# Optimization experiments

Hardware: AMD Instinct MI355X
Metric: run time of the kernel (lower is better)

## Reference

```python
import jax, jax.numpy as jnp
import numpy as np

LAMBDAS = (1.0, 10.0)
MAX_NEURONS = 12
RECONFIG = 50
INIT_BATCH = 4000
BATCH_INC = 2166
NS = 2  # switch point: normal equations -> QR -> incremental QR


def setup_inputs() -> dict:
    key = jax.random.key(0)
    kx, ky = jax.random.split(key)
    X = jax.random.normal(kx, (30000, 784), dtype=jnp.float32)
    labels = jax.random.randint(ky, (30000,), 0, 10)
    Y = jax.nn.one_hot(labels, 10, dtype=jnp.float32)  # [N, 10] one-hot targets
    return {"X": X, "Y": Y}


def _forward(X, Y, key):
    N, d = X.shape
    n_cand = len(LAMBDAS) * RECONFIG
    lam = jnp.repeat(jnp.asarray(LAMBDAS, dtype=X.dtype), RECONFIG)  # [n_cand]
    H = jnp.zeros((N, MAX_NEURONS), dtype=X.dtype)
    W = jnp.zeros((d, 0), dtype=X.dtype)
    b = jnp.zeros((0,), dtype=X.dtype)
    Q = R = QT = beta = None
    y = Y
    batch_size = INIT_BATCH
    for k in range(MAX_NEURONS):
        key, kperm, kw, kb = jax.random.split(key, 4)
        indices = jax.random.permutation(kperm, N)[:batch_size]
        Xk = X[indices]              # [B, d]
        Tk = Y[indices]              # [B, 10]
        ek = Tk if k == 0 else Tk - y[indices]  # residual on the batch
        # candidate random features, scaled per-lambda
        W_random = lam * (2.0 * jax.random.uniform(kw, (d, n_cand), dtype=X.dtype) - 1.0)
        b_random = lam * (2.0 * jax.random.uniform(kb, (1, n_cand), dtype=X.dtype) - 1.0)
        h = jax.nn.sigmoid(Xk @ W_random + b_random)             # [B, n_cand]
        v = (ek.T @ h) ** 2 / jnp.sum(h * h, axis=0)             # [10, n_cand]
        best = jnp.argmax(jnp.mean(v, axis=0))
        W_c = jax.lax.dynamic_slice_in_dim(W_random, best, 1, axis=1)  # [d, 1]
        b_c = jax.lax.dynamic_slice_in_dim(b_random, best, 1, axis=1)[0]  # [1]
        h_c = jax.nn.sigmoid(X @ W_c + b_c)[:, 0]                # [N]
        H = H.at[:, k].set(h_c)
        W = jnp.concatenate([W, W_c], axis=1)
        b = jnp.concatenate([b, b_c], axis=0)
        Hk = H[:, : k + 1]
        if k < NS:
            beta = jnp.linalg.inv(Hk.T @ Hk) @ (Hk.T @ Y)
        elif k == NS:
            Q, R = jnp.linalg.qr(Hk)
            QT = Q.T @ Y
            beta = jax.scipy.linalg.solve_triangular(R, QT, lower=False)
        else:
            # incremental Gram-Schmidt QR update with the new column h_c
            r1 = Q.T @ h_c                       # [k]
            t = h_c - Q @ r1
            r2 = jnp.linalg.norm(t)
            q = t / r2
            Q = jnp.concatenate([Q, q[:, None]], axis=1)
            R = jnp.block([[R, r1[:, None]],
                           [jnp.zeros((1, k), R.dtype), r2[None, None]]])
            QT = jnp.concatenate([QT, (q @ Y)[None, :]], axis=0)
            beta = jax.scipy.linalg.solve_triangular(R, QT, lower=False)
        y = Hk @ beta
        batch_size += BATCH_INC
    return W, b, beta


def reference(X, Y):
    return _forward(X, Y, jax.random.key(42))
```

## Files before the change

kernel.cpp:

```cpp
#include <hip/hip_runtime.h>
#include <cstdint>
#include <cstddef>
#include <cmath>

#define N_ROWS 30000
#define D_IN   784
#define NC     100
#define NCP    128
#define NSEG   12
#define SEG    30000
#define SORT_BLOCKS 118
#define KP     800
#define MAXBLK 435
#define SL     16

typedef short bf16x8 __attribute__((ext_vector_type(8)));
typedef float f32x4  __attribute__((ext_vector_type(4)));

struct Hdr {
  uint32_t kperm[12][2];
  uint32_t kw[12][2];
  uint32_t kb[12][2];
  uint32_t sub[12][2][2];
  int best; int pad0;
  float bsel;
  float r2arr[12];
  float r1s[12 * SL];
  float r1bs[12 * SL];
  float R[144];
  float QT[120];
  float beta[120];
  float den[100];
  float num[1000];
};

__device__ __forceinline__ void tf2x32(uint32_t k0, uint32_t k1,
                                       uint32_t x0, uint32_t x1,
                                       uint32_t& o0, uint32_t& o1) {
  const uint32_t kx = k0 ^ k1 ^ 0x1BD11BDAu;
  x0 += k0; x1 += k1;
  x0 += x1; x1 = (x1<<13)|(x1>>19); x1 ^= x0;
  x0 += x1; x1 = (x1<<15)|(x1>>17); x1 ^= x0;
  x0 += x1; x1 = (x1<<26)|(x1>>6);  x1 ^= x0;
  x0 += x1; x1 = (x1<<6) |(x1>>26); x1 ^= x0;
  x0 += k1; x1 += kx + 1u;
  x0 += x1; x1 = (x1<<17)|(x1>>15); x1 ^= x0;
  x0 += x1; x1 = (x1<<29)|(x1>>3);  x1 ^= x0;
  x0 += x1; x1 = (x1<<16)|(x1>>16); x1 ^= x0;
  x0 += x1; x1 = (x1<<24)|(x1>>8);  x1 ^= x0;
  x0 += kx; x1 += k0 + 2u;
  x0 += x1; x1 = (x1<<13)|(x1>>19); x1 ^= x0;
  x0 += x1; x1 = (x1<<15)|(x1>>17); x1 ^= x0;
  x0 += x1; x1 = (x1<<26)|(x1>>6);  x1 ^= x0;
  x0 += x1; x1 = (x1<<6) |(x1>>26); x1 ^= x0;
  x0 += k0; x1 += k1 + 3u;
  x0 += x1; x1 = (x1<<17)|(x1>>15); x1 ^= x0;
  x0 += x1; x1 = (x1<<29)|(x1>>3);  x1 ^= x0;
  x0 += x1; x1 = (x1<<16)|(x1>>16); x1 ^= x0;
  x0 += x1; x1 = (x1<<24)|(x1>>8);  x1 ^= x0;
  x0 += k1; x1 += kx + 4u;
  x0 += x1; x1 = (x1<<13)|(x1>>19); x1 ^= x0;
  x0 += x1; x1 = (x1<<15)|(x1>>17); x1 ^= x0;
  x0 += x1; x1 = (x1<<26)|(x1>>6);  x1 ^= x0;
  x0 += x1; x1 = (x1<<6) |(x1>>26); x1 ^= x0;
  x0 += kx; x1 += k0 + 5u;
  o0 = x0; o1 = x1;
}

__device__ __forceinline__ float u01(uint32_t bits) {
  return __uint_as_float((bits >> 9) | 0x3f800000u) - 1.0f;
}

__device__ __forceinline__ uint32_t rbits32(uint32_t k0, uint32_t k1, uint32_t idx) {
  uint32_t o0, o1;
  tf2x32(k0, k1, 0u, idx, o0, o1);
  return o0 ^ o1;
}

__device__ __forceinline__ ushort f2bf_rne(float f) {
  uint32_t u = __float_as_uint(f);
  return (ushort)((u + 0x7fffu + ((u >> 16) & 1u)) >> 16);
}
__device__ __forceinline__ float bf2f(ushort h) {
  return __uint_as_float(((uint32_t)h) << 16);
}

__global__ void k_rng_chain(Hdr* h) {
  if (threadIdx.x != 0 || blockIdx.x != 0) return;
  uint32_t c0 = 0u, c1 = 42u;
  for (int k = 0; k < 12; k++) {
    uint32_t t0, t1;
    tf2x32(c0, c1, 0u, 1u, t0, t1); h->kperm[k][0] = t0; h->kperm[k][1] = t1;
    tf2x32(c0, c1, 0u, 2u, t0, t1); h->kw[k][0]   = t0; h->kw[k][1]   = t1;
    tf2x32(c0, c1, 0u, 3u, t0, t1); h->kb[k][0]   = t0; h->kb[k][1]   = t1;
    uint32_t p0 = h->kperm[k][0], p1 = h->kperm[k][1];
    for (int r = 0; r < 2; r++) {
      uint32_t s0, s1, n0, n1;
      tf2x32(p0, p1, 0u, 1u, s0, s1);
      tf2x32(p0, p1, 0u, 0u, n0, n1);
      h->sub[k][r][0] = s0; h->sub[k][r][1] = s1;
      p0 = n0; p1 = n1;
    }
    tf2x32(c0, c1, 0u, 0u, t0, t1); c0 = t0; c1 = t1;
  }
}

__global__ __launch_bounds__(256) void k_sortkeys(const Hdr* __restrict__ h,
    uint32_t* __restrict__ keys, int* __restrict__ vals, int round) {
  int p = blockIdx.x * 256 + threadIdx.x;
  if (p >= NSEG * SEG) return;
  int s = p / SEG, i = p % SEG;
  keys[p] = rbits32(h->sub[s][round][0], h->sub[s][round][1], (uint32_t)i);
  if (round == 0) vals[p] = i;
}

__global__ __launch_bounds__(256) void k_hist(const uint32_t* __restrict__ keys,
    uint32_t* __restrict__ hs, int shift) {
  __shared__ uint32_t hloc[256];
  int s = blockIdx.x / SORT_BLOCKS, b = blockIdx.x % SORT_BLOCKS;
  hloc[threadIdx.x] = 0;
  __syncthreads();
  int i = b * 256 + threadIdx.x;
  if (i < SEG) {
    uint32_t d = (keys[s * SEG + i] >> shift) & 255u;
    atomicAdd(&hloc[d], 1u);
  }
  __syncthreads();
  hs[(size_t)(s * SORT_BLOCKS + b) * 256 + threadIdx.x] = hloc[threadIdx.x];
}

__global__ __launch_bounds__(256) void k_scan(uint32_t* hs, uint32_t* baseA) {
  __shared__ uint32_t tot[256];
  __shared__ uint32_t base[256];
  int s = blockIdx.x, d = threadIdx.x;
  uint32_t run = 0;
  uint32_t buf[30];
  for (int c0 = 0; c0 < SORT_BLOCKS; c0 += 30) {
    int n = SORT_BLOCKS - c0; if (n > 30) n = 30;
    #pragma unroll
    for (int j = 0; j < 30; j++)
      if (j < n) buf[j] = hs[(size_t)(s * SORT_BLOCKS + c0 + j) * 256 + d];
    #pragma unroll
    for (int j = 0; j < 30; j++)
      if (j < n) {
        uint32_t c = buf[j];
        hs[(size_t)(s * SORT_BLOCKS + c0 + j) * 256 + d] = run;
        run += c;
      }
  }
  tot[d] = run;
  __syncthreads();
  if (d == 0) {
    uint32_t acc = 0;
    for (int q = 0; q < 256; q++) { base[q] = acc; acc += tot[q]; }
  }
  __syncthreads();
  baseA[s * 256 + d] = base[d];
}

__global__ __launch_bounds__(256) void k_scatter(const uint32_t* __restrict__ ik,
    const int* __restrict__ iv, uint32_t* __restrict__ ok, int* __restrict__ ov,
    const uint32_t* __restrict__ hs, const uint32_t* __restrict__ baseA, int shift) {
  __shared__ uint16_t wh[4][256];
  int s = blockIdx.x / SORT_BLOCKS, b = blockIdx.x % SORT_BLOCKS;
  int tid = threadIdx.x;
  for (int q = tid; q < 1024; q += 256) ((uint16_t*)wh)[q] = 0;
  __syncthreads();
  int i = b * 256 + tid;
  bool valid = (i < SEG);
  uint32_t key = 0, dg = 0; int val = 0;
  if (valid) {
    key = ik[s * SEG + i];
    val = iv[s * SEG + i];
    dg = (key >> shift) & 255u;
  }
  unsigned long long vm = __ballot(valid ? 1 : 0);
  unsigned long long m = ~0ULL;
  for (int bit = 0; bit < 8; bit++) {
    unsigned long long bm = __ballot((int)((dg >> bit) & 1u));
    m &= ((dg >> bit) & 1u) ? bm : ~bm;
  }
  m &= vm;
  int wv = tid >> 6, lane = tid & 63;
  int rw = __popcll(m & ((1ULL << lane) - 1ULL));
  if (valid && rw == 0) wh[wv][dg] = (uint16_t)__popcll(m);
  __syncthreads();
  if (valid) {
    int rank = rw;
    for (int q = 0; q < wv; q++) rank += wh[q][dg];
    uint32_t pos = hs[(size_t)(s * SORT_BLOCKS + b) * 256 + dg] + baseA[s * 256 + dg] + rank;
    ok[s * SEG + pos] = key;
    ov[s * SEG + pos] = val;
  }
}

__global__ __launch_bounds__(256) void k_gen(const Hdr* __restrict__ h,
    float* __restrict__ Wr, short* __restrict__ Wthi, short* __restrict__ Wtlo) {
  int t = blockIdx.x * 256 + threadIdx.x;
  if (t >= NSEG * NCP * KP) return;
  int seg = t / (NCP * KP);
  int r = t % (NCP * KP);
  int c = r / KP, d = r % KP;
  float val = 0.f;
  if (c < NC && d < D_IN) {
    int n = d * NC + c;
    float u = u01(rbits32(h->kw[seg][0], h->kw[seg][1], (uint32_t)n));
    float lam = (c < 50) ? 1.f : 10.f;
    val = lam * (2.f * u - 1.f);
  }
  ushort hi = f2bf_rne(val);
  ushort lo = f2bf_rne(val - bf2f(hi));
  Wthi[t] = (short)hi;
  Wtlo[t] = (short)lo;
  if (d < D_IN) Wr[(size_t)seg * D_IN * NCP + (size_t)d * NCP + c] = val;
}

__global__ __launch_bounds__(256) void k_genb(const Hdr* __restrict__ h, float* __restrict__ br) {
  int t = blockIdx.x * 256 + threadIdx.x;
  if (t >= NSEG * NC) return;
  int k = t / NC, c = t % NC;
  float u = u01(rbits32(h->kb[k][0], h->kb[k][1], (uint32_t)c));
  float lam = (c < 50) ? 1.f : 10.f;
  br[t] = lam * (2.f * u - 1.f);
}

__global__ __launch_bounds__(256) void k_batch_mfma(const float* __restrict__ X,
    const short* __restrict__ Wthi, const short* __restrict__ Wtlo,
    const float* __restrict__ br, const int* __restrict__ perm,
    const float* __restrict__ Y, const float* __restrict__ Hbuf,
    const Hdr* __restrict__ hd, float* __restrict__ P, int kk, int bs) {
  __shared__ short Ah[64][40], Al[64][40];
  __shared__ short Bh[128][40], Bl[128][40];
  __shared__ int idxs[64];
  __shared__ float ekS[64][10];
  __shared__ float hS[64][12];
  __shared__ float betaS[120];
  int tid = threadIdx.x;
  int row0 = blockIdx.x * 64;
  if (tid < 64) {
    int rr = row0 + tid;
    idxs[tid] = perm[rr < bs ? rr : (bs - 1)];
  }
  if (kk > 0 && tid < kk * 10) betaS[tid] = hd->beta[tid];
  __syncthreads();
  if (kk > 0) {
    for (int q = tid; q < 64 * kk; q += 256) {
      int r = q / kk, m = q % kk;
      hS[r][m] = Hbuf[(size_t)idxs[r] * 12 + m];
    }
  }
  __syncthreads();
  for (int q = tid; q < 640; q += 256) {
    int r = q / 10, j = q % 10;
    float e = 0.f;
    if (row0 + r < bs) {
      e = Y[(size_t)idxs[r] * 10 + j];
      if (kk > 0) {
        float yv = 0.f;
        for (int m = 0; m < kk; m++) yv += hS[r][m] * betaS[m * 10 + j];
        e -= yv;
      }
    }
    ekS[r][j] = e;
  }
  int wave = tid >> 6, lane = tid & 63;
  int kg = lane >> 4, ln = lane & 15;

  f32x4 acc[4][2];
  #pragma unroll
  for (int m = 0; m < 4; m++)
    #pragma unroll
    for (int j = 0; j < 2; j++)
      acc[m][j] = (f32x4){0.f, 0.f, 0.f, 0.f};

  int arow = tid >> 2, aq = tid & 3;
  int bcol = tid >> 1, bh2 = tid & 1;

  for (int k0 = 0; k0 < KP; k0 += 32) {
    __syncthreads();
    {
      int kbase = k0 + aq * 8;
      const float* xr = X + (size_t)idxs[arow] * D_IN;
      float v[8];
      if (kbase + 8 <= D_IN) {
        float4 p0 = *(const float4*)(xr + kbase);
        float4 p1 = *(const float4*)(xr + kbase + 4);
        v[0]=p0.x; v[1]=p0.y; v[2]=p0.z; v[3]=p0.w;
        v[4]=p1.x; v[5]=p1.y; v[6]=p1.z; v[7]=p1.w;
      } else {
        #pragma unroll
        for (int q = 0; q < 8; q++) v[q] = (kbase + q < D_IN) ? xr[kbase + q] : 0.f;
      }
      uint32_t ph[4], pl[4];
      #pragma unroll
      for (int q = 0; q < 4; q++) {
        ushort h0 = f2bf_rne(v[2*q]),   h1 = f2bf_rne(v[2*q+1]);
        ushort l0 = f2bf_rne(v[2*q]   - bf2f(h0));
        ushort l1 = f2bf_rne(v[2*q+1] - bf2f(h1));
        ph[q] = (uint32_t)h0 | ((uint32_t)h1 << 16);
        pl[q] = (uint32_t)l0 | ((uint32_t)l1 << 16);
      }
      *(uint4*)&Ah[arow][aq*8] = make_uint4(ph[0], ph[1], ph[2], ph[3]);
      *(uint4*)&Al[arow][aq*8] = make_uint4(pl[0], pl[1], pl[2], pl[3]);
    }
    {
      int boff = bh2 * 16;
      const uint4* sh = (const uint4*)(Wthi + (size_t)bcol * KP + k0 + boff);
      const uint4* sl = (const uint4*)(Wtlo + (size_t)bcol * KP + k0 + boff);
      uint4 h0 = sh[0], h1 = sh[1], l0 = sl[0], l1 = sl[1];
      *(uint4*)&Bh[bcol][boff]     = h0;
      *(uint4*)&Bh[bcol][boff + 8] = h1;
      *(uint4*)&Bl[bcol][boff]     = l0;
      *(uint4*)&Bl[bcol][boff + 8] = l1;
    }
    __syncthreads();
    bf16x8 bhf[2], blf[2];
    #pragma unroll
    for (int j = 0; j < 2; j++) {
      int n = (2 * wave + j) * 16 + ln;
      bhf[j] = *(bf16x8*)&Bh[n][kg * 8];
      blf[j] = *(bf16x8*)&Bl[n][kg * 8];
    }
    #pragma unroll
    for (int m = 0; m < 4; m++) {
      bf16x8 ah = *(bf16x8*)&Ah[m * 16 + ln][kg * 8];
      bf16x8 al = *(bf16x8*)&Al[m * 16 + ln][kg * 8];
      #pragma unroll
      for (int j = 0; j < 2; j++) {
        acc[m][j] = __builtin_amdgcn_mfma_f32_16x16x32_bf16(ah, bhf[j], acc[m][j], 0, 0, 0);
        acc[m][j] = __builtin_amdgcn_mfma_f32_16x16x32_bf16(ah, blf[j], acc[m][j], 0, 0, 0);
        acc[m][j] = __builtin_amdgcn_mfma_f32_16x16x32_bf16(al, bhf[j], acc[m][j], 0, 0, 0);
      }
    }
  }
  #pragma unroll
  for (int j = 0; j < 2; j++) {
    int col = (2 * wave + j) * 16 + ln;
    float bias = (col < NC) ? br[col] : 0.f;
    float den_t = 0.f;
    float num_t[10];
    #pragma unroll
    for (int q = 0; q < 10; q++) num_t[q] = 0.f;
    #pragma unroll
    for (int m = 0; m < 4; m++) {
      #pragma unroll
      for (int r = 0; r < 4; r++) {
        int rl = m * 16 + kg * 4 + r;
        if (row0 + rl < bs) {
          float hsig = 1.f / (1.f + expf(-(acc[m][j][r] + bias)));
          den_t += hsig * hsig;
          #pragma unroll
          for (int q = 0; q < 10; q++) num_t[q] += hsig * ekS[rl][q];
        }
      }
    }
    den_t += __shfl_xor(den_t, 16, 64);
    den_t += __shfl_xor(den_t, 32, 64);
    #pragma unroll
    for (int q = 0; q < 10; q++) {
      num_t[q] += __shfl_xor(num_t[q], 16, 64);
      num_t[q] += __shfl_xor(num_t[q], 32, 64);
    }
    if (kg == 0 && col < NC) {
      float* dst = P + (size_t)blockIdx.x * 1100 + col * 11;
      dst[0] = den_t;
      #pragma unroll
      for (int q = 0; q < 10; q++) dst[1 + q] = num_t[q];
    }
  }
}

__global__ __launch_bounds__(256) void k_score_select(const float* __restrict__ P,
    Hdr* h, const float* __restrict__ brk, const float* __restrict__ Wr,
    float* __restrict__ wcol, float* __restrict__ outW, float* __restrict__ outB,
    int* __restrict__ ticket, int k, int nblk) {
  int c = blockIdx.x;
  int tid = threadIdx.x;
  int q = tid % 11, g = tid / 11;
  float acc = 0.f;
  if (tid < 253) {
    for (int b = g; b < nblk; b += 23)
      acc += P[(size_t)b * 1100 + c * 11 + q];
  }
  __shared__ float red[23][11];
  if (tid < 253) red[g][q] = acc;
  __syncthreads();
  if (tid < 11) {
    float s = 0.f;
    #pragma unroll
    for (int g2 = 0; g2 < 23; g2++) s += red[g2][tid];
    if (tid == 0) h->den[c] = s;
    else h->num[c * 10 + tid - 1] = s;
  }
  __shared__ int sdone;
  __syncthreads();
  __threadfence();
  if (tid == 0) {
    int old = atomicAdd(ticket, 1);
    sdone = (old == NC - 1) ? 1 : 0;
  }
  __syncthreads();
  if (!sdone) return;
  __threadfence();
  __shared__ int sbest;
  if (tid < 12 * SL) { h->r1s[tid] = 0.f; h->r1bs[tid] = 0.f; }
  if (tid == 0) {
    float best = -1.f; int bi = 0;
    for (int cc = 0; cc < NC; cc++) {
      float s = 0.f;
      for (int j = 0; j < 10; j++) { float n = h->num[cc * 10 + j]; s += n * n; }
      float v = s / (h->den[cc] * 10.f);
      if (v > best) { best = v; bi = cc; }
    }
    h->best = bi;
    h->bsel = brk[bi];
    outB[k] = h->bsel;
    sbest = bi;
  }
  __syncthreads();
  int best = sbest;
  for (int d = tid; d < D_IN; d += 256) {
    float v = Wr[(size_t)d * NCP + best];
    wcol[d] = v;
    outW[d * 12 + k] = v;
  }
}

__global__ __launch_bounds__(256) void k_hc(const float* __restrict__ X,
    const Hdr* __restrict__ h, const float* __restrict__ wcol,
    float* __restrict__ H, float* __restrict__ hc, int k) {
  int lane = threadIdx.x & 63;
  int row = blockIdx.x * 4 + (threadIdx.x >> 6);
  if (row >= N_ROWS) return;
  const float4* xp = (const float4*)(X + (size_t)row * D_IN);
  const float4* wp = (const float4*)wcol;
  float acc = 0.f;
  #pragma unroll
  for (int it = 0; it < 4; it++) {
    int p = lane + it * 64;
    if (p < 196) {
      float4 xv = xp[p], wv = wp[p];
      acc += xv.x * wv.x + xv.y * wv.y + xv.z * wv.z + xv.w * wv.w;
    }
  }
  #pragma unroll
  for (int o = 32; o > 0; o >>= 1) acc += __shfl_xor(acc, o, 64);
  if (lane == 0) {
    float hv = 1.f / (1.f + expf(-(acc + h->bsel)));
    H[(size_t)row * 12 + k] = hv;
    hc[row] = hv;
  }
}

__global__ __launch_bounds__(256) void k_dotQ(const float* __restrict__ Tcm,
    const float* __restrict__ vec, float* __restrict__ dst) {
  int j = blockIdx.x / SL, sl = blockIdx.x % SL;
  const float* q = Tcm + (size_t)j * N_ROWS;
  int i0 = sl * (N_ROWS / SL);
  int i1 = i0 + (N_ROWS / SL);
  float a = 0.f;
  for (int i = i0 + threadIdx.x; i < i1; i += 256) a += q[i] * vec[i];
  __shared__ float red[256];
  red[threadIdx.x] = a;
  __syncthreads();
  for (int s = 128; s > 0; s >>= 1) {
    if (threadIdx.x < s) red[threadIdx.x] += red[threadIdx.x + s];
    __syncthreads();
  }
  if (threadIdx.x == 0) dst[j * SL + sl] = red[0];
}

__global__ __launch_bounds__(256) void k_sub_fin(Hdr* h, float* __restrict__ Tcm,
    const float* __restrict__ basev, const float* __restrict__ coefp,
    const float* __restrict__ Y, float* __restrict__ partials,
    float* __restrict__ out_beta, int* __restrict__ ticket, int k, int dofin) {
  __shared__ float cf[12];
  int tid = threadIdx.x;
  if (tid < 12) {
    float s = 0.f;
    #pragma unroll
    for (int s8 = 0; s8 < SL; s8++) s += coefp[tid * SL + s8];
    float r2j = (tid < k) ? h->r2arr[tid] : 1.f;
    cf[tid] = s / (r2j * r2j);
  }
  __syncthreads();
  int i = blockIdx.x * 256 + tid;
  float t = 0.f;
  float v[11];
  #pragma unroll
  for (int q = 0; q < 11; q++) v[q] = 0.f;
  if (i < N_ROWS) {
    t = basev[i];
    for (int j = 0; j < k; j++) t -= Tcm[(size_t)j * N_ROWS + i] * cf[j];
    Tcm[(size_t)k * N_ROWS + i] = t;
    if (dofin) {
      const float* yr = Y + (size_t)i * 10;
      #pragma unroll
      for (int q = 0; q < 10; q++) v[q] = t * yr[q];
      v[10] = t * t;
    }
  }
  if (!dofin) return;
  #pragma unroll
  for (int o = 1; o < 64; o <<= 1) {
    #pragma unroll
    for (int q = 0; q < 11; q++) v[q] += __shfl_xor(v[q], o, 64);
  }
  __shared__ float wred[4][11];
  int wave = tid >> 6, lane = tid & 63;
  if (lane == 0) {
    #pragma unroll
    for (int q = 0; q < 11; q++) wred[wave][q] = v[q];
  }
  __syncthreads();
  if (tid < 11) {
    float s = wred[0][tid] + wred[1][tid] + wred[2][tid] + wred[3][tid];
    partials[blockIdx.x * 12 + tid] = s;
  }
  __shared__ int sdone;
  __syncthreads();
  __threadfence();
  if (tid == 0) {
    int old = atomicAdd(ticket, 1);
    sdone = (old == SORT_BLOCKS - 1) ? 1 : 0;
  }
  __syncthreads();
  if (!sdone) return;
  __threadfence();
  __shared__ float red[23][11];
  int q = tid % 11, g = tid / 11;
  float acc2 = 0.f;
  if (tid < 253) {
    for (int b = g; b < SORT_BLOCKS; b += 23)
      acc2 += partials[b * 12 + q];
  }
  if (tid < 253) red[g][q] = acc2;
  __syncthreads();
  __shared__ float s[11];
  __shared__ float Rcol[12];
  __shared__ float r2s;
  if (tid < 11) {
    float ss = 0.f;
    #pragma unroll
    for (int g2 = 0; g2 < 23; g2++) ss += red[g2][tid];
    s[tid] = ss;
  }
  __syncthreads();
  if (tid == 0) {
    float r2 = sqrtf(s[10]);
    h->r2arr[k] = r2;
    h->R[k * 12 + k] = r2;
    r2s = r2;
    Rcol[k] = r2;
    for (int i2 = 0; i2 < k; i2++) {
      float rs = 0.f;
      #pragma unroll
      for (int s8 = 0; s8 < SL; s8++) rs += h->r1s[i2 * SL + s8] + h->r1bs[i2 * SL + s8];
      float Rik = rs / h->r2arr[i2];
      h->R[i2 * 12 + k] = Rik;
      Rcol[i2] = Rik;
    }
  }
  __syncthreads();
  if (tid < 10) {
    float qtk = s[tid] / r2s;
    h->QT[k * 10 + tid] = qtk;
    float bloc[12];
    for (int i2 = k; i2 >= 0; i2--) {
      float t2 = (i2 == k) ? qtk : h->QT[i2 * 10 + tid];
      for (int m = i2 + 1; m <= k; m++) {
        float Rim = (m == k) ? Rcol[i2] : h->R[i2 * 12 + m];
        t2 -= Rim * bloc[m];
      }
      t2 /= ((i2 == k) ? r2s : h->R[i2 * 12 + i2]);
      bloc[i2] = t2;
      h->beta[i2 * 10 + tid] = t2;
      out_beta[i2 * 10 + tid] = t2;
    }
  }
}

static inline int cdiv(int a, int b) { return (a + b - 1) / b; }

extern "C" void kernel_launch(void* const* d_in, const int* in_sizes, int n_in,
                              void* d_out, int out_size, void* d_ws, size_t ws_size,
                              hipStream_t stream) {
  const float* X = (const float*)d_in[0];
  const float* Y = (const float*)d_in[1];
  float* out = (float*)d_out;
  float* outW = out;
  float* outB = out + 9408;
  float* outBeta = out + 9420;

  char* base = (char*)d_ws;
  Hdr* hdr = (Hdr*)base;
  float* r1p  = (float*)(base + offsetof(Hdr, r1s));
  float* r1bp = (float*)(base + offsetof(Hdr, r1bs));

  size_t off = 16384;
  auto nxt = [&](size_t bytes) -> void* {
    void* p = base + off;
    off += (bytes + 255) & ~(size_t)255;
    return p;
  };
  int* tickets = (int*)nxt(256);
  uint32_t* keysA = (uint32_t*)nxt((size_t)NSEG * SEG * 4);
  uint32_t* keysB = (uint32_t*)nxt((size_t)NSEG * SEG * 4);
  int* valsA = (int*)nxt((size_t)NSEG * SEG * 4);
  int* valsB = (int*)nxt((size_t)NSEG * SEG * 4);
  uint32_t* hs = (uint32_t*)nxt((size_t)NSEG * SORT_BLOCKS * 256 * 4);
  uint32_t* baseA = (uint32_t*)nxt((size_t)NSEG * 256 * 4);
  float* WrAll = (float*)nxt((size_t)NSEG * D_IN * NCP * 4);
  short* WthiAll = (short*)nxt((size_t)NSEG * NCP * KP * 2);
  short* WtloAll = (short*)nxt((size_t)NSEG * NCP * KP * 2);
  float* brAll = (float*)nxt((size_t)NSEG * NC * 4);
  float* wcol = (float*)nxt((size_t)D_IN * 4);
  float* Pbuf = (float*)nxt((size_t)MAXBLK * 1100 * 4);
  float* Tcm = (float*)nxt((size_t)12 * N_ROWS * 4);
  float* Hbuf = (float*)nxt((size_t)N_ROWS * 12 * 4);
  float* hcbuf = (float*)nxt((size_t)N_ROWS * 4);
  float* partials = (float*)nxt(128 * 12 * 4);

  hipMemsetAsync(tickets, 0, 256, stream);

  k_rng_chain<<<1, 64, 0, stream>>>(hdr);

  const int keygrid = cdiv(NSEG * SEG, 256);
  const int sortgrid = NSEG * SORT_BLOCKS;
  for (int round = 0; round < 2; round++) {
    k_sortkeys<<<keygrid, 256, 0, stream>>>(hdr, keysA, valsA, round);
    for (int pass = 0; pass < 4; pass++) {
      uint32_t* ik = (pass & 1) ? keysB : keysA;
      uint32_t* ok = (pass & 1) ? keysA : keysB;
      int* iv = (pass & 1) ? valsB : valsA;
      int* ov = (pass & 1) ? valsA : valsB;
      k_hist<<<sortgrid, 256, 0, stream>>>(ik, hs, 8 * pass);
      k_scan<<<NSEG, 256, 0, stream>>>(hs, baseA);
      k_scatter<<<sortgrid, 256, 0, stream>>>(ik, iv, ok, ov, hs, baseA, 8 * pass);
    }
  }

  k_gen<<<cdiv(NSEG * NCP * KP, 256), 256, 0, stream>>>(hdr, WrAll, WthiAll, WtloAll);
  k_genb<<<cdiv(NSEG * NC, 256), 256, 0, stream>>>(hdr, brAll);

  for (int k = 0; k < 12; k++) {
    int bs = 4000 + 2166 * k;
    int nblk = cdiv(bs, 64);
    const int* perm = valsA + (size_t)k * SEG;
    const short* Wthi = WthiAll + (size_t)k * NCP * KP;
    const short* Wtlo = WtloAll + (size_t)k * NCP * KP;
    const float* brk = brAll + (size_t)k * NC;

    k_batch_mfma<<<nblk, 256, 0, stream>>>(X, Wthi, Wtlo, brk, perm, Y, Hbuf, hdr, Pbuf, k, bs);
    k_score_select<<<NC, 256, 0, stream>>>(Pbuf, hdr, brk,
        WrAll + (size_t)k * D_IN * NCP, wcol, outW, outB, &tickets[k], k, nblk);
    k_hc<<<7500, 256, 0, stream>>>(X, hdr, wcol, Hbuf, hcbuf, k);
    if (k > 0) k_dotQ<<<k * SL, 256, 0, stream>>>(Tcm, hcbuf, r1p);
    if (k == 1 || k == 2) {
      k_sub_fin<<<SORT_BLOCKS, 256, 0, stream>>>(hdr, Tcm, hcbuf, r1p, Y, partials,
          outBeta, &tickets[32 + k], k, 0);
      k_dotQ<<<k * SL, 256, 0, stream>>>(Tcm, Tcm + (size_t)k * N_ROWS, r1bp);
      k_sub_fin<<<SORT_BLOCKS, 256, 0, stream>>>(hdr, Tcm, Tcm + (size_t)k * N_ROWS, r1bp,
          Y, partials, outBeta, &tickets[32 + k], k, 1);
    } else {
      k_sub_fin<<<SORT_BLOCKS, 256, 0, stream>>>(hdr, Tcm, hcbuf, r1p, Y, partials,
          outBeta, &tickets[32 + k], k, 1);
    }
  }
}
```

Baseline: 1.647 ms.

## Presplit X to bf16 hi/lo once; fuse radix-sort key gen, histogram and scan

X is now split into bf16 hi/lo pairs once by a dedicated kernel, and the batch MFMA kernel loads those pairs directly instead of re-splitting gathered rows on every call. The radix sort merges key generation with the first histogram, and folds each per-segment scan into the histogram kernel through a last-block ticket. The bias generation kernel is merged into the weight generator. Together these remove repeated conversion arithmetic and several kernel launches, at the cost of an extra 96 MB of hi/lo buffers and threadfence/atomic ticket synchronisation.

```diff
diff --git a/kernel.cpp b/kernel.cpp
--- a/kernel.cpp
+++ b/kernel.cpp
@@ -105,34 +105,40 @@
   }
 }
 
-__global__ __launch_bounds__(256) void k_sortkeys(const Hdr* __restrict__ h,
-    uint32_t* __restrict__ keys, int* __restrict__ vals, int round) {
-  int p = blockIdx.x * 256 + threadIdx.x;
-  if (p >= NSEG * SEG) return;
-  int s = p / SEG, i = p % SEG;
-  keys[p] = rbits32(h->sub[s][round][0], h->sub[s][round][1], (uint32_t)i);
-  if (round == 0) vals[p] = i;
-}
-
-__global__ __launch_bounds__(256) void k_hist(const uint32_t* __restrict__ keys,
-    uint32_t* __restrict__ hs, int shift) {
-  __shared__ uint32_t hloc[256];
-  int s = blockIdx.x / SORT_BLOCKS, b = blockIdx.x % SORT_BLOCKS;
-  hloc[threadIdx.x] = 0;
-  __syncthreads();
-  int i = b * 256 + threadIdx.x;
-  if (i < SEG) {
-    uint32_t d = (keys[s * SEG + i] >> shift) & 255u;
-    atomicAdd(&hloc[d], 1u);
-  }
-  __syncthreads();
-  hs[(size_t)(s * SORT_BLOCKS + b) * 256 + threadIdx.x] = hloc[threadIdx.x];
-}
-
-__global__ __launch_bounds__(256) void k_scan(uint32_t* hs, uint32_t* baseA) {
+__global__ __launch_bounds__(256) void k_splitX(const float* __restrict__ X,
+    short* __restrict__ Xhi, short* __restrict__ Xlo) {
+  int t = blockIdx.x * 256 + threadIdx.x;
+  if (t >= N_ROWS * (KP / 8)) return;
+  int i = t / (KP / 8), g = t % (KP / 8);
+  int kb = g * 8;
+  float v[8];
+  if (kb + 8 <= D_IN) {
+    const float* xr = X + (size_t)i * D_IN + kb;
+    float4 p0 = *(const float4*)xr;
+    float4 p1 = *(const float4*)(xr + 4);
+    v[0]=p0.x; v[1]=p0.y; v[2]=p0.z; v[3]=p0.w;
+    v[4]=p1.x; v[5]=p1.y; v[6]=p1.z; v[7]=p1.w;
+  } else {
+    #pragma unroll
+    for (int q = 0; q < 8; q++) v[q] = 0.f;
+  }
+  uint32_t ph[4], pl[4];
+  #pragma unroll
+  for (int q = 0; q < 4; q++) {
+    ushort h0 = f2bf_rne(v[2*q]),   h1 = f2bf_rne(v[2*q+1]);
+    ushort l0 = f2bf_rne(v[2*q]   - bf2f(h0));
+    ushort l1 = f2bf_rne(v[2*q+1] - bf2f(h1));
+    ph[q] = (uint32_t)h0 | ((uint32_t)h1 << 16);
+    pl[q] = (uint32_t)l0 | ((uint32_t)l1 << 16);
+  }
+  size_t o = (size_t)i * KP + kb;
+  *(uint4*)(Xhi + o) = make_uint4(ph[0], ph[1], ph[2], ph[3]);
+  *(uint4*)(Xlo + o) = make_uint4(pl[0], pl[1], pl[2], pl[3]);
+}
+
+__device__ __forceinline__ void scan_segment(uint32_t* hs, uint32_t* baseA, int s, int d) {
   __shared__ uint32_t tot[256];
   __shared__ uint32_t base[256];
-  int s = blockIdx.x, d = threadIdx.x;
   uint32_t run = 0;
   uint32_t buf[30];
   for (int c0 = 0; c0 < SORT_BLOCKS; c0 += 30) {
@@ -156,6 +162,57 @@
   }
   __syncthreads();
   baseA[s * 256 + d] = base[d];
+}
+
+__global__ __launch_bounds__(256) void k_keys_hist(const Hdr* __restrict__ h,
+    uint32_t* __restrict__ keys, int* __restrict__ vals,
+    uint32_t* __restrict__ hs, uint32_t* __restrict__ baseA,
+    int* __restrict__ tick, int round) {
+  __shared__ uint32_t hloc[256];
+  int s = blockIdx.x / SORT_BLOCKS, b = blockIdx.x % SORT_BLOCKS;
+  int tid = threadIdx.x;
+  hloc[tid] = 0;
+  __syncthreads();
+  int i = b * 256 + tid;
+  if (i < SEG) {
+    uint32_t key = rbits32(h->sub[s][round][0], h->sub[s][round][1], (uint32_t)i);
+    keys[s * SEG + i] = key;
+    if (round == 0) vals[s * SEG + i] = i;
+    atomicAdd(&hloc[key & 255u], 1u);
+  }
+  __syncthreads();
+  hs[(size_t)(s * SORT_BLOCKS + b) * 256 + tid] = hloc[tid];
+  __shared__ int sdone;
+  __threadfence();
+  if (tid == 0) sdone = (atomicAdd(&tick[s], 1) == SORT_BLOCKS - 1) ? 1 : 0;
+  __syncthreads();
+  if (!sdone) return;
+  __threadfence();
+  scan_segment(hs, baseA, s, tid);
+}
+
+__global__ __launch_bounds__(256) void k_hist_scan(const uint32_t* __restrict__ keys,
+    uint32_t* __restrict__ hs, uint32_t* __restrict__ baseA,
+    int* __restrict__ tick, int shift) {
+  __shared__ uint32_t hloc[256];
+  int s = blockIdx.x / SORT_BLOCKS, b = blockIdx.x % SORT_BLOCKS;
+  int tid = threadIdx.x;
+  hloc[tid] = 0;
+  __syncthreads();
+  int i = b * 256 + tid;
+  if (i < SEG) {
+    uint32_t d = (keys[s * SEG + i] >> shift) & 255u;
+    atomicAdd(&hloc[d], 1u);
+  }
+  __syncthreads();
+  hs[(size_t)(s * SORT_BLOCKS + b) * 256 + tid] = hloc[tid];
+  __shared__ int sdone;
+  __threadfence();
+  if (tid == 0) sdone = (atomicAdd(&tick[s], 1) == SORT_BLOCKS - 1) ? 1 : 0;
+  __syncthreads();
+  if (!sdone) return;
+  __threadfence();
+  scan_segment(hs, baseA, s, tid);
 }
 
 __global__ __launch_bounds__(256) void k_scatter(const uint32_t* __restrict__ ik,
@@ -195,9 +252,16 @@
 }
 
 __global__ __launch_bounds__(256) void k_gen(const Hdr* __restrict__ h,
-    float* __restrict__ Wr, short* __restrict__ Wthi, short* __restrict__ Wtlo) {
+    float* __restrict__ Wr, short* __restrict__ Wthi, short* __restrict__ Wtlo,
+    float* __restrict__ br) {
   int t = blockIdx.x * 256 + threadIdx.x;
   if (t >= NSEG * NCP * KP) return;
+  if (t < NSEG * NC) {
+    int k = t / NC, c = t % NC;
+    float u = u01(rbits32(h->kb[k][0], h->kb[k][1], (uint32_t)c));
+    float lam = (c < 50) ? 1.f : 10.f;
+    br[t] = lam * (2.f * u - 1.f);
+  }
   int seg = t / (NCP * KP);
   int r = t % (NCP * KP);
   int c = r / KP, d = r % KP;
@@ -215,16 +279,8 @@
   if (d < D_IN) Wr[(size_t)seg * D_IN * NCP + (size_t)d * NCP + c] = val;
 }
 
-__global__ __launch_bounds__(256) void k_genb(const Hdr* __restrict__ h, float* __restrict__ br) {
-  int t = blockIdx.x * 256 + threadIdx.x;
-  if (t >= NSEG * NC) return;
-  int k = t / NC, c = t % NC;
-  float u = u01(rbits32(h->kb[k][0], h->kb[k][1], (uint32_t)c));
-  float lam = (c < 50) ? 1.f : 10.f;
-  br[t] = lam * (2.f * u - 1.f);
-}
-
-__global__ __launch_bounds__(256) void k_batch_mfma(const float* __restrict__ X,
+__global__ __launch_bounds__(256) void k_batch_mfma(const short* __restrict__ Xhi,
+    const short* __restrict__ Xlo,
     const short* __restrict__ Wthi, const short* __restrict__ Wtlo,
     const float* __restrict__ br, const int* __restrict__ perm,
     const float* __restrict__ Y, const float* __restrict__ Hbuf,
@@ -279,29 +335,9 @@
   for (int k0 = 0; k0 < KP; k0 += 32) {
     __syncthreads();
     {
-      int kbase = k0 + aq * 8;
-      const float* xr = X + (size_t)idxs[arow] * D_IN;
-      float v[8];
-      if (kbase + 8 <= D_IN) {
-        float4 p0 = *(const float4*)(xr + kbase);
-        float4 p1 = *(const float4*)(xr + kbase + 4);
-        v[0]=p0.x; v[1]=p0.y; v[2]=p0.z; v[3]=p0.w;
-        v[4]=p1.x; v[5]=p1.y; v[6]=p1.z; v[7]=p1.w;
-      } else {
-        #pragma unroll
-        for (int q = 0; q < 8; q++) v[q] = (kbase + q < D_IN) ? xr[kbase + q] : 0.f;
-      }
-      uint32_t ph[4], pl[4];
-      #pragma unroll
-      for (int q = 0; q < 4; q++) {
-        ushort h0 = f2bf_rne(v[2*q]),   h1 = f2bf_rne(v[2*q+1]);
-        ushort l0 = f2bf_rne(v[2*q]   - bf2f(h0));
-        ushort l1 = f2bf_rne(v[2*q+1] - bf2f(h1));
-        ph[q] = (uint32_t)h0 | ((uint32_t)h1 << 16);
-        pl[q] = (uint32_t)l0 | ((uint32_t)l1 << 16);
-      }
-      *(uint4*)&Ah[arow][aq*8] = make_uint4(ph[0], ph[1], ph[2], ph[3]);
-      *(uint4*)&Al[arow][aq*8] = make_uint4(pl[0], pl[1], pl[2], pl[3]);
+      size_t o = (size_t)idxs[arow] * KP + k0 + aq * 8;
+      *(uint4*)&Ah[arow][aq * 8] = *(const uint4*)(Xhi + o);
+      *(uint4*)&Al[arow][aq * 8] = *(const uint4*)(Xlo + o);
     }
     {
       int boff = bh2 * 16;
@@ -603,7 +639,7 @@
     off += (bytes + 255) & ~(size_t)255;
     return p;
   };
-  int* tickets = (int*)nxt(256);
+  int* tickets = (int*)nxt(1024);
   uint32_t* keysA = (uint32_t*)nxt((size_t)NSEG * SEG * 4);
   uint32_t* keysB = (uint32_t*)nxt((size_t)NSEG * SEG * 4);
   int* valsA = (int*)nxt((size_t)NSEG * SEG * 4);
@@ -620,28 +656,30 @@
   float* Hbuf = (float*)nxt((size_t)N_ROWS * 12 * 4);
   float* hcbuf = (float*)nxt((size_t)N_ROWS * 4);
   float* partials = (float*)nxt(128 * 12 * 4);
-
-  hipMemsetAsync(tickets, 0, 256, stream);
+  short* Xhi = (short*)nxt((size_t)N_ROWS * KP * 2);
+  short* Xlo = (short*)nxt((size_t)N_ROWS * KP * 2);
+
+  hipMemsetAsync(tickets, 0, 1024, stream);
 
   k_rng_chain<<<1, 64, 0, stream>>>(hdr);
-
-  const int keygrid = cdiv(NSEG * SEG, 256);
+  k_splitX<<<cdiv(N_ROWS * (KP / 8), 256), 256, 0, stream>>>(X, Xhi, Xlo);
+
   const int sortgrid = NSEG * SORT_BLOCKS;
   for (int round = 0; round < 2; round++) {
-    k_sortkeys<<<keygrid, 256, 0, stream>>>(hdr, keysA, valsA, round);
-    for (int pass = 0; pass < 4; pass++) {
+    int* tkbase = tickets + 64 + round * 48;
+    k_keys_hist<<<sortgrid, 256, 0, stream>>>(hdr, keysA, valsA, hs, baseA, tkbase, round);
+    k_scatter<<<sortgrid, 256, 0, stream>>>(keysA, valsA, keysB, valsB, hs, baseA, 0);
+    for (int pass = 1; pass < 4; pass++) {
       uint32_t* ik = (pass & 1) ? keysB : keysA;
       uint32_t* ok = (pass & 1) ? keysA : keysB;
       int* iv = (pass & 1) ? valsB : valsA;
       int* ov = (pass & 1) ? valsA : valsB;
-      k_hist<<<sortgrid, 256, 0, stream>>>(ik, hs, 8 * pass);
-      k_scan<<<NSEG, 256, 0, stream>>>(hs, baseA);
+      k_hist_scan<<<sortgrid, 256, 0, stream>>>(ik, hs, baseA, tkbase + pass * 12, 8 * pass);
       k_scatter<<<sortgrid, 256, 0, stream>>>(ik, iv, ok, ov, hs, baseA, 8 * pass);
     }
   }
 
-  k_gen<<<cdiv(NSEG * NCP * KP, 256), 256, 0, stream>>>(hdr, WrAll, WthiAll, WtloAll);
-  k_genb<<<cdiv(NSEG * NC, 256), 256, 0, stream>>>(hdr, brAll);
+  k_gen<<<cdiv(NSEG * NCP * KP, 256), 256, 0, stream>>>(hdr, WrAll, WthiAll, WtloAll, brAll);
 
   for (int k = 0; k < 12; k++) {
     int bs = 4000 + 2166 * k;
@@ -651,7 +689,7 @@
     const short* Wtlo = WtloAll + (size_t)k * NCP * KP;
     const float* brk = brAll + (size_t)k * NC;
 
-    k_batch_mfma<<<nblk, 256, 0, stream>>>(X, Wthi, Wtlo, brk, perm, Y, Hbuf, hdr, Pbuf, k, bs);
+    k_batch_mfma<<<nblk, 256, 0, stream>>>(Xhi, Xlo, Wthi, Wtlo, brk, perm, Y, Hbuf, hdr, Pbuf, k, bs);
     k_score_select<<<NC, 256, 0, stream>>>(Pbuf, hdr, brk,
         WrAll + (size_t)k * D_IN * NCP, wcol, outW, outB, &tickets[k], k, nblk);
     k_hc<<<7500, 256, 0, stream>>>(X, hdr, wcol, Hbuf, hcbuf, k);
```

After: 2.452 ms. 48.8% more time.
